# Kernel optimization log

Measured on AMD Instinct MI355X. Metric: run time of the kernel, lower is better.

The kernel has to match this reference:

```python
import jax, jax.numpy as jnp
import numpy as np

# Pangu-Weather EarthSpecificBlock, layer-1 config
WZ, WH, WW = 2, 6, 12          # window size (z, lat, lon)
Z, H, W = 8, 91, 180           # token grid after patch embedding
C = 192                        # token dim
HEADS = 6
B = 1
PAD_TOP, PAD_BOT = 2, 3        # lat 91 -> 96 (CustomPad3d, centered)
ZP, HP, WP = 8, 96, 180        # padded grid
NWB = (ZP // WZ) * (HP // WH)  # 64 bias windows (z*lat)
N = WZ * WH * WW               # 144 tokens per window


def earth_position_index():
    zi = np.arange(WZ); zj = -np.arange(WZ) * WZ
    hi = np.arange(WH); hj = -np.arange(WH) * WH
    w = np.arange(WW)
    c1 = np.stack(np.meshgrid(zi, hi, w, indexing='ij')).reshape(3, -1)
    c2 = np.stack(np.meshgrid(zj, hj, w, indexing='ij')).reshape(3, -1)
    coords = (c1[:, :, None] - c2[:, None, :]).transpose(1, 2, 0).astype(np.int64)
    coords[:, :, 2] += WW - 1
    coords[:, :, 1] *= 2 * WW - 1
    coords[:, :, 0] *= (2 * WW - 1) * WH * WH
    return coords.sum(-1)  # (N, N) int indices into bias table

POS_IDX = jnp.asarray(earth_position_index())


def layer_norm(x, w, b, eps=1e-5):
    mu = x.mean(-1, keepdims=True)
    var = ((x - mu) ** 2).mean(-1, keepdims=True)
    return (x - mu) * jax.lax.rsqrt(var + eps) * w + b


def setup_inputs() -> dict:
    key = jax.random.key(0)
    ks = jax.random.split(key, 8)
    f = lambda k, s: jax.random.normal(k, s, jnp.float32) * 0.02
    return {
        "x": jax.random.normal(ks[0], (B, Z * H * W, C), jnp.float32),
        "qkv_w": f(ks[1], (3 * C, C)),
        "qkv_b": jnp.zeros((3 * C,), jnp.float32),
        "proj_w": f(ks[2], (C, C)),
        "proj_b": jnp.zeros((C,), jnp.float32),
        "bias_table": f(ks[3], ((2 * WW - 1) * WH * WH * WZ * WZ, NWB, HEADS)),
        "norm1_w": jnp.ones((C,), jnp.float32),
        "norm1_b": jnp.zeros((C,), jnp.float32),
        "norm2_w": jnp.ones((C,), jnp.float32),
        "norm2_b": jnp.zeros((C,), jnp.float32),
        "mlp_w1": f(ks[4], (4 * C, C)),
        "mlp_b1": jnp.zeros((4 * C,), jnp.float32),
        "mlp_w2": f(ks[5], (C, 4 * C)),
        "mlp_b2": jnp.zeros((C,), jnp.float32),
        "roll": 0,
    }


def reference(x, qkv_w, qkv_b, proj_w, proj_b, bias_table,
              norm1_w, norm1_b, norm2_w, norm2_b,
              mlp_w1, mlp_b1, mlp_w2, mlp_b2, roll):
    shortcut = x  # (B, L, C)
    hd = C // HEADS
    scale = hd ** -0.5
    xs = x.reshape(B, Z, H, W, C)
    xs = jnp.pad(xs, ((0, 0), (0, 0), (PAD_TOP, PAD_BOT), (0, 0), (0, 0)))
    # window partition: (B, ZP, HP, WP, C) -> (nb, N, C), windows ordered (z, lat, lon)
    xw = xs.reshape(B, ZP // WZ, WZ, HP // WH, WH, WP // WW, WW, C)
    xw = xw.transpose(0, 1, 3, 5, 2, 4, 6, 7).reshape(-1, N, C)
    nb = xw.shape[0]  # B * 64 * 15 = 960
    qkv = (xw @ qkv_w.T + qkv_b).reshape(nb, N, 3, HEADS, hd).transpose(2, 0, 3, 1, 4)
    q, k, v = qkv[0] * scale, qkv[1], qkv[2]  # each (nb, HEADS, N, hd)
    att = jnp.einsum('bhnd,bhmd->bhnm', q, k)  # (nb, HEADS, N, N)
    # earth-specific bias gathered via position index
    bias = bias_table[POS_IDX]                 # (N, N, NWB, HEADS)
    bias = bias.transpose(2, 3, 0, 1)          # (NWB, HEADS, N, N)
    # nb = B * NWB * n_lon_windows, NWB is the leading window factor
    att = att.reshape(B, NWB, -1, HEADS, N, N) + bias[None, :, None]
    att = jax.nn.softmax(att, axis=-1).reshape(nb, HEADS, N, N)
    out = jnp.einsum('bhnm,bhmd->bnhd', att, v).reshape(nb, N, C)
    out = out @ proj_w.T + proj_b
    # window reverse + crop padding
    out = out.reshape(B, ZP // WZ, HP // WH, WP // WW, WZ, WH, WW, C)
    out = out.transpose(0, 1, 4, 2, 5, 3, 6, 7).reshape(B, ZP, HP, WP, C)
    out = out[:, :, PAD_TOP:HP - PAD_BOT, :, :].reshape(B, -1, C)
    # post-norm residual (Pangu): x = shortcut + norm1(attn); x = x + norm2(mlp(x))
    x1 = shortcut + layer_norm(out, norm1_w, norm1_b)
    h1 = jax.nn.gelu(x1 @ mlp_w1.T + mlp_b1, approximate=False)
    mlp_out = h1 @ mlp_w2.T + mlp_b2
    return x1 + layer_norm(mlp_out, norm2_w, norm2_b)
```

## Files before the change

### kernel.cpp

```cpp
#include <hip/hip_runtime.h>
#include <hip/hip_bf16.h>

typedef __hip_bfloat16 bf16;
#define DEVI __device__ __forceinline__

typedef __bf16 bf16x8 __attribute__((ext_vector_type(8)));
typedef __bf16 bf16x4 __attribute__((ext_vector_type(4)));
typedef float  f32x4  __attribute__((ext_vector_type(4)));

DEVI float bf2f(bf16 v) { return __bfloat162float(v); }
DEVI bf16 f2bf(float v) { return __float2bfloat16(v); }

DEVI unsigned short bfbits(float x) {
    bf16 h = __float2bfloat16(x);
    return *reinterpret_cast<unsigned short*>(&h);
}
DEVI unsigned int pack2(float x, float y) {
    return (unsigned int)bfbits(x) | ((unsigned int)bfbits(y) << 16);
}
DEVI bf16x8 pack8(float4 lo, float4 hi) {
    union { unsigned int u[4]; bf16x8 v; } z;
    z.u[0] = pack2(lo.x, lo.y); z.u[1] = pack2(lo.z, lo.w);
    z.u[2] = pack2(hi.x, hi.y); z.u[3] = pack2(hi.z, hi.w);
    return z.v;
}
DEVI bf16x8 ld8h(const bf16* p) {
    bf16x4 lo = *(const bf16x4*)p;
    bf16x4 hi = *(const bf16x4*)(p + 4);
    return __builtin_shufflevector(lo, hi, 0, 1, 2, 3, 4, 5, 6, 7);
}

__global__ __launch_bounds__(256) void prep_attn_w(
    const float* __restrict__ qkv_w, const float* __restrict__ qkv_b,
    bf16* __restrict__ qkv_wb, float* __restrict__ qkv_bb)
{
    const float scale = 0.17677669529663687f;
    int idx = blockIdx.x * 256 + threadIdx.x;
    if (idx < 110592) {
        int c = idx % 192, d = idx / 192;
        int h = d / 96, q2 = d - h * 96, seg = q2 >> 5, rr = q2 & 31;
        float v = qkv_w[(size_t)(seg * 192 + h * 32 + rr) * 192 + c];
        if (seg == 0) v *= scale;
        qkv_wb[idx] = f2bf(v);
    }
    if (idx < 576) {
        int h = idx / 96, q2 = idx - h * 96, seg = q2 >> 5, rr = q2 & 31;
        float b = qkv_b[seg * 192 + h * 32 + rr];
        if (seg == 0) b *= scale;
        qkv_bb[idx] = b;
    }
}

__global__ __launch_bounds__(256) void prep_bias(
    const float* __restrict__ bias_table, bf16* __restrict__ biasT)
{
    int idx = blockIdx.x * 256 + threadIdx.x;
    if (idx >= 7962624) return;
    int t = idx % 144;
    int k = (idx / 144) % 144;
    int r2 = idx / 20736;
    int h = r2 % 6, wb = r2 / 6;
    int tzq = t / 72, thq = (t / 12) % 6, twq = t % 12;
    int tzk = k / 72, thk = (k / 12) % 6, twk = k % 12;
    int bidx = (tzq + 2 * tzk) * 828 + (thq + 6 * thk) * 23 + (twq - twk + 11);
    biasT[idx] = f2bf(bias_table[(size_t)(bidx * 64 + wb) * 6 + h]);
}

__global__ __launch_bounds__(256, 3) void attn_mfma_kernel(
    const float* __restrict__ x, const bf16* __restrict__ qkv_wb,
    const float* __restrict__ qkv_bb, const bf16* __restrict__ biasT,
    bf16* __restrict__ attn_out)
{
    __shared__ alignas(16) char sm[30976];
    bf16* Qs  = (bf16*)sm;
    bf16* Ks  = (bf16*)(sm + 10368);
    bf16* VTs = (bf16*)(sm + 20736);

    const int tid  = threadIdx.x;
    const int wave = tid >> 6;
    const int lane = tid & 63;
    const int quad = lane >> 4;
    const int l15  = lane & 15;

    const int bid     = blockIdx.x;
    const int logical = (bid & 7) * 720 + (bid >> 3);
    const int wi      = logical / 6;
    const int head    = logical % 6;
    const int ww_  = wi % 15;
    const int hw   = (wi / 15) % 16;
    const int zw   = wi / 240;
    const int wb   = zw * 16 + hw;

    for (int i = tid; i < 512; i += 256) {
        int d = i >> 4, c = i & 15;
        VTs[d * 160 + 144 + c] = f2bf(0.f);
    }

    bf16x8 af[3][6];
#pragma unroll
    for (int i = 0; i < 3; ++i) {
        int mt = wave + 4 * i;
        if (mt < 9) {
            int t  = mt * 16 + l15;
            int tz = t / 72, rr = t - tz * 72;
            int th = rr / 12, tw = rr - th * 12;
            int lat = hw * 6 + th - 2;
            bool valid = (lat >= 0 && lat < 91);
            size_t base = ((size_t)((zw * 2 + tz) * 91 + (valid ? lat : 0)) * 180
                           + ww_ * 12 + tw) * 192;
#pragma unroll
            for (int ks = 0; ks < 6; ++ks) {
                float4 lo = make_float4(0.f, 0.f, 0.f, 0.f);
                float4 hi = make_float4(0.f, 0.f, 0.f, 0.f);
                if (valid) {
                    lo = *(const float4*)(x + base + ks * 32 + quad * 8);
                    hi = *(const float4*)(x + base + ks * 32 + quad * 8 + 4);
                }
                af[i][ks] = pack8(lo, hi);
            }
        }
    }

    for (int nt = 0; nt < 6; ++nt) {
        const bf16* wrow = qkv_wb + (size_t)(head * 96 + nt * 16 + l15) * 192;
        bf16x8 bw[6];
#pragma unroll
        for (int ks = 0; ks < 6; ++ks)
            bw[ks] = *(const bf16x8*)(wrow + ks * 32 + quad * 8);
        float bias = qkv_bb[head * 96 + nt * 16 + l15];

        f32x4 acc[3];
#pragma unroll
        for (int i = 0; i < 3; ++i) acc[i] = (f32x4){0.f, 0.f, 0.f, 0.f};
#pragma unroll
        for (int ks = 0; ks < 6; ++ks)
#pragma unroll
            for (int i = 0; i < 3; ++i) {
                int mt = wave + 4 * i;
                if (mt < 9)
                    acc[i] = __builtin_amdgcn_mfma_f32_16x16x32_bf16(
                        af[i][ks], bw[ks], acc[i], 0, 0, 0);
            }
#pragma unroll
        for (int i = 0; i < 3; ++i) {
            int mt = wave + 4 * i;
            if (mt < 9) {
#pragma unroll
                for (int r = 0; r < 4; ++r) {
                    float v = acc[i][r] + bias;
                    int tok = mt * 16 + quad * 4 + r;
                    if (nt < 2)      Qs[tok * 36 + nt * 16 + l15] = f2bf(v);
                    else if (nt < 4) Ks[tok * 36 + (nt - 2) * 16 + l15] = f2bf(v);
                    else             VTs[((nt - 4) * 16 + l15) * 160 + tok] = f2bf(v);
                }
            }
        }
    }
    __syncthreads();

    bf16x8 qb[3];
#pragma unroll
    for (int i = 0; i < 3; ++i) {
        int nti = wave + 4 * i;
        if (nti < 9) qb[i] = ld8h(Qs + (nti * 16 + l15) * 36 + quad * 8);
    }
    f32x4 st[3][9];
#pragma unroll
    for (int mt = 0; mt < 9; ++mt) {
        bf16x8 ka = ld8h(Ks + (mt * 16 + l15) * 36 + quad * 8);
#pragma unroll
        for (int i = 0; i < 3; ++i) {
            int nti = wave + 4 * i;
            st[i][mt] = (f32x4){0.f, 0.f, 0.f, 0.f};
            if (nti < 9)
                st[i][mt] = __builtin_amdgcn_mfma_f32_16x16x32_bf16(
                    ka, qb[i], st[i][mt], 0, 0, 0);
        }
    }

    const bf16* bt = biasT + (size_t)(wb * 6 + head) * 20736;
#pragma unroll
    for (int i = 0; i < 3; ++i) {
        int nti = wave + 4 * i;
        if (nti < 9) {
#pragma unroll
            for (int mt = 0; mt < 9; ++mt)
#pragma unroll
                for (int r = 0; r < 4; ++r)
                    st[i][mt][r] += bf2f(bt[(mt * 16 + quad * 4 + r) * 144
                                            + nti * 16 + l15]);
        }
    }

#pragma unroll
    for (int i = 0; i < 3; ++i) {
        int nti = wave + 4 * i;
        if (nti < 9) {
            float mx = -1e30f;
#pragma unroll
            for (int mt = 0; mt < 9; ++mt)
#pragma unroll
                for (int r = 0; r < 4; ++r) mx = fmaxf(mx, st[i][mt][r]);
            mx = fmaxf(mx, __shfl_xor(mx, 16, 64));
            mx = fmaxf(mx, __shfl_xor(mx, 32, 64));
            float s = 0.f;
#pragma unroll
            for (int mt = 0; mt < 9; ++mt)
#pragma unroll
                for (int r = 0; r < 4; ++r) {
                    float e = __expf(st[i][mt][r] - mx);
                    st[i][mt][r] = e;
                    s += e;
                }
            s += __shfl_xor(s, 16, 64);
            s += __shfl_xor(s, 32, 64);
            float inv = 1.f / s;
#pragma unroll
            for (int mt = 0; mt < 9; ++mt)
#pragma unroll
                for (int r = 0; r < 4; ++r) st[i][mt][r] *= inv;
        }
    }

    f32x4 oa[3][2];
#pragma unroll
    for (int i = 0; i < 3; ++i)
#pragma unroll
        for (int n2 = 0; n2 < 2; ++n2) oa[i][n2] = (f32x4){0.f, 0.f, 0.f, 0.f};

#pragma unroll
    for (int i = 0; i < 3; ++i) {
        int nti = wave + 4 * i;
        if (nti < 9) {
#pragma unroll
            for (int ks = 0; ks < 5; ++ks) {
                unsigned A0 = pack2(st[i][2 * ks][0], st[i][2 * ks][1]);
                unsigned A1 = pack2(st[i][2 * ks][2], st[i][2 * ks][3]);
                unsigned B0 = 0u, B1 = 0u;
                if (ks < 4) {
                    B0 = pack2(st[i][2 * ks + 1][0], st[i][2 * ks + 1][1]);
                    B1 = pack2(st[i][2 * ks + 1][2], st[i][2 * ks + 1][3]);
                }
                bool lo2 = quad < 2;
                unsigned Z0 = lo2 ? A0 : B0, Z1 = lo2 ? A1 : B1;
                unsigned Y0 = lo2 ? B0 : A0, Y1 = lo2 ? B1 : A1;
                unsigned s16_0 = __shfl_xor((int)Z0, 16, 64);
                unsigned s16_1 = __shfl_xor((int)Z1, 16, 64);
                unsigned s32_0 = __shfl_xor((int)Y0, 32, 64);
                unsigned s32_1 = __shfl_xor((int)Y1, 32, 64);
                unsigned s48_0 = __shfl_xor((int)Y0, 48, 64);
                unsigned s48_1 = __shfl_xor((int)Y1, 48, 64);
                union { unsigned u[4]; bf16x8 v; } fr;
                fr.u[0] = (quad == 0) ? Z0 : (quad == 1) ? s48_0 : (quad == 2) ? s32_0 : s16_0;
                fr.u[1] = (quad == 0) ? Z1 : (quad == 1) ? s48_1 : (quad == 2) ? s32_1 : s16_1;
                fr.u[2] = (quad == 0) ? s16_0 : (quad == 1) ? s32_0 : (quad == 2) ? s48_0 : Z0;
                fr.u[3] = (quad == 0) ? s16_1 : (quad == 1) ? s32_1 : (quad == 2) ? s48_1 : Z1;
#pragma unroll
                for (int n2 = 0; n2 < 2; ++n2) {
                    bf16x8 vb = *(const bf16x8*)(VTs + (n2 * 16 + l15) * 160
                                                 + ks * 32 + quad * 8);
                    oa[i][n2] = __builtin_amdgcn_mfma_f32_16x16x32_bf16(
                        fr.v, vb, oa[i][n2], 0, 0, 0);
                }
            }
        }
    }

#pragma unroll
    for (int i = 0; i < 3; ++i) {
        int nti = wave + 4 * i;
        if (nti < 9) {
#pragma unroll
            for (int n2 = 0; n2 < 2; ++n2)
#pragma unroll
                for (int r = 0; r < 4; ++r) {
                    int tok = nti * 16 + quad * 4 + r;
                    attn_out[(size_t)(wi * 144 + tok) * 192 + (head << 5) + n2 * 16 + l15]
                        = f2bf(oa[i][n2][r]);
                }
        }
    }
}

__global__ __launch_bounds__(256, 2) void proj_mfma_kernel(
    const bf16* __restrict__ attn, const float* __restrict__ proj_w,
    const float* __restrict__ proj_b, const float* __restrict__ xin,
    const float* __restrict__ n1w, const float* __restrict__ n1b,
    bf16* __restrict__ x1out)
{
    __shared__ alignas(16) char sm[56320];
    bf16*  Xs     = (bf16*)sm;
    float* wsum   = (float*)(sm + 51200);
    float* wsq    = (float*)(sm + 53248);
    float* mean_s = (float*)(sm + 55296);
    float* rstd_s = (float*)(sm + 55808);

    const int tid  = threadIdx.x;
    const int wave = tid >> 6;
    const int lane = tid & 63;
    const int quad = lane >> 4;
    const int l15  = lane & 15;
    const long tok0 = (long)blockIdx.x * 128;
    const int colw = wave * 48;

    for (int i = tid; i < 128 * 24; i += 256) {
        int r = i / 24, c4 = i - r * 24;
        long l = tok0 + r;
        uint4 v = make_uint4(0u, 0u, 0u, 0u);
        if (l < 131040) {
            int li  = (int)l;
            int z   = li / 16380, rem = li - z * 16380;
            int lat = rem / 180, lon = rem - lat * 180;
            int latp = lat + 2;
            int zw = z >> 1, tz = z & 1;
            int hw = latp / 6, th = latp - hw * 6;
            int wwn = lon / 12, tw = lon - wwn * 12;
            int wi = (zw * 16 + hw) * 15 + wwn;
            int t  = (tz * 6 + th) * 12 + tw;
            v = *(const uint4*)(attn + (size_t)(wi * 144 + t) * 192 + c4 * 8);
        }
        *(uint4*)(Xs + r * 200 + c4 * 8) = v;
    }
    __syncthreads();

    f32x4 o[3][8];
#pragma unroll
    for (int nt = 0; nt < 3; ++nt)
#pragma unroll
        for (int mt = 0; mt < 8; ++mt)
            o[nt][mt] = (f32x4){0.f, 0.f, 0.f, 0.f};

#pragma unroll
    for (int ks = 0; ks < 6; ++ks) {
        bf16x8 wfr[3];
#pragma unroll
        for (int nt = 0; nt < 3; ++nt) {
            const float* wp = proj_w + (size_t)(colw + nt * 16 + l15) * 192
                            + ks * 32 + quad * 8;
            float4 lo = *(const float4*)wp;
            float4 hi = *(const float4*)(wp + 4);
            wfr[nt] = pack8(lo, hi);
        }
#pragma unroll
        for (int mt = 0; mt < 8; ++mt) {
            bf16x8 a = *(const bf16x8*)(Xs + (mt * 16 + l15) * 200 + ks * 32 + quad * 8);
#pragma unroll
            for (int nt = 0; nt < 3; ++nt)
                o[nt][mt] = __builtin_amdgcn_mfma_f32_16x16x32_bf16(
                    a, wfr[nt], o[nt][mt], 0, 0, 0);
        }
    }

    float pbv[3], gw[3], gb[3];
#pragma unroll
    for (int nt = 0; nt < 3; ++nt) {
        int c = colw + nt * 16 + l15;
        pbv[nt] = proj_b[c];
        gw[nt]  = n1w[c];
        gb[nt]  = n1b[c];
    }
#pragma unroll
    for (int nt = 0; nt < 3; ++nt)
#pragma unroll
        for (int mt = 0; mt < 8; ++mt)
#pragma unroll
            for (int r = 0; r < 4; ++r)
                o[nt][mt][r] += pbv[nt];

#pragma unroll
    for (int mt = 0; mt < 8; ++mt) {
#pragma unroll
        for (int r = 0; r < 4; ++r) {
            float p = o[0][mt][r] + o[1][mt][r] + o[2][mt][r];
            float q = o[0][mt][r] * o[0][mt][r] + o[1][mt][r] * o[1][mt][r]
                    + o[2][mt][r] * o[2][mt][r];
#pragma unroll
            for (int m_ = 1; m_ < 16; m_ <<= 1) {
                p += __shfl_xor(p, m_, 64);
                q += __shfl_xor(q, m_, 64);
            }
            if (l15 == 0) {
                int row = mt * 16 + quad * 4 + r;
                wsum[row * 4 + wave] = p;
                wsq [row * 4 + wave] = q;
            }
        }
    }
    __syncthreads();
    if (tid < 128) {
        float s  = wsum[tid * 4] + wsum[tid * 4 + 1] + wsum[tid * 4 + 2] + wsum[tid * 4 + 3];
        float ss = wsq [tid * 4] + wsq [tid * 4 + 1] + wsq [tid * 4 + 2] + wsq [tid * 4 + 3];
        float m = s * (1.f / 192.f);
        float var = ss * (1.f / 192.f) - m * m;
        mean_s[tid] = m;
        rstd_s[tid] = rsqrtf(fmaxf(var, 0.f) + 1e-5f);
    }
    __syncthreads();

#pragma unroll
    for (int mt = 0; mt < 8; ++mt) {
#pragma unroll
        for (int r = 0; r < 4; ++r) {
            int row = mt * 16 + quad * 4 + r;
            long tok = tok0 + row;
            if (tok < 131040) {
                float m = mean_s[row], rsd = rstd_s[row];
#pragma unroll
                for (int nt = 0; nt < 3; ++nt) {
                    int c = colw + nt * 16 + l15;
                    float val = (o[nt][mt][r] - m) * rsd * gw[nt] + gb[nt]
                              + xin[(size_t)tok * 192 + c];
                    x1out[(size_t)tok * 192 + c] = f2bf(val);
                }
            }
        }
    }
}

__global__ __launch_bounds__(256) void prep_weights(
    const float* __restrict__ w1, const float* __restrict__ w2,
    unsigned int* __restrict__ w1b, unsigned int* __restrict__ w2b)
{
    int i = blockIdx.x * 256 + threadIdx.x;
    if (i < 73728) {
        w1b[i] = pack2(w1[2 * i], w1[2 * i + 1]);
    } else {
        int j = i - 73728;
        w2b[j] = pack2(w2[2 * j], w2[2 * j + 1]);
    }
}

__global__ __launch_bounds__(256, 2) void mlp_mfma_kernel(
    const bf16* __restrict__ x1, const bf16* __restrict__ w1b,
    const float* __restrict__ b1, const bf16* __restrict__ w2b,
    const float* __restrict__ b2, const float* __restrict__ n2w,
    const float* __restrict__ n2b, float* __restrict__ out)
{
    __shared__ alignas(16) char sm[53760];
    bf16*  Xs     = (bf16*)sm;
    bf16*  Hs     = (bf16*)(sm + 25600);
    float* wsum   = (float*)(sm + 51200);
    float* wsq    = (float*)(sm + 52224);
    float* mean_s = (float*)(sm + 53248);
    float* rstd_s = (float*)(sm + 53504);

    const int tid  = threadIdx.x;
    const int wave = tid >> 6;
    const int lane = tid & 63;
    const int quad = lane >> 4;
    const int l15  = lane & 15;
    const long tok0 = (long)blockIdx.x * 64;
    const int colw = wave * 48;

    for (int i = tid; i < 64 * 24; i += 256) {
        int r = i / 24, c8 = i - r * 24;
        uint4 v = make_uint4(0u, 0u, 0u, 0u);
        if (tok0 + r < 131040)
            v = *(const uint4*)(x1 + (tok0 + r) * 192 + (size_t)c8 * 8);
        *(uint4*)(Xs + r * 200 + c8 * 8) = v;
    }
    __syncthreads();

    bf16x8 af[4][6];
#pragma unroll
    for (int mt = 0; mt < 4; ++mt)
#pragma unroll
        for (int ks = 0; ks < 6; ++ks)
            af[mt][ks] = *(const bf16x8*)(Xs + (mt * 16 + l15) * 200 + ks * 32 + quad * 8);

    f32x4 o[3][4];
#pragma unroll
    for (int nt = 0; nt < 3; ++nt)
#pragma unroll
        for (int mt = 0; mt < 4; ++mt)
            o[nt][mt] = (f32x4){0.f, 0.f, 0.f, 0.f};

    for (int nc = 0; nc < 4; ++nc) {
        f32x4 g[3][4];
#pragma unroll
        for (int nt = 0; nt < 3; ++nt)
#pragma unroll
            for (int mt = 0; mt < 4; ++mt)
                g[nt][mt] = (f32x4){0.f, 0.f, 0.f, 0.f};
        const int h0 = nc * 192 + colw;
#pragma unroll
        for (int ks = 0; ks < 6; ++ks) {
            bf16x8 bfr[3];
#pragma unroll
            for (int nt = 0; nt < 3; ++nt)
                bfr[nt] = *(const bf16x8*)(w1b + (size_t)(h0 + nt * 16 + l15) * 192 + ks * 32 + quad * 8);
#pragma unroll
            for (int nt = 0; nt < 3; ++nt)
#pragma unroll
                for (int mt = 0; mt < 4; ++mt)
                    g[nt][mt] = __builtin_amdgcn_mfma_f32_16x16x32_bf16(
                        af[mt][ks], bfr[nt], g[nt][mt], 0, 0, 0);
        }
        __syncthreads();

#pragma unroll
        for (int nt = 0; nt < 3; ++nt) {
            float bb = b1[h0 + nt * 16 + l15];
            int hcol = colw + nt * 16 + l15;
#pragma unroll
            for (int mt = 0; mt < 4; ++mt) {
#pragma unroll
                for (int r = 0; r < 4; ++r) {
                    float v = g[nt][mt][r] + bb;
                    float u = v * (0.7978845608028654f + 0.035677408136300125f * v * v);
                    float e = __expf(2.f * u);
                    float t = 1.f - 2.f / (e + 1.f);
                    float gl = 0.5f * v * (1.f + t);
                    Hs[(mt * 16 + quad * 4 + r) * 200 + hcol] = f2bf(gl);
                }
            }
        }
        __syncthreads();

#pragma unroll
        for (int ks = 0; ks < 6; ++ks) {
            bf16x8 hf[4];
#pragma unroll
            for (int mt = 0; mt < 4; ++mt)
                hf[mt] = *(const bf16x8*)(Hs + (mt * 16 + l15) * 200 + ks * 32 + quad * 8);
            bf16x8 wf[3];
#pragma unroll
            for (int nt = 0; nt < 3; ++nt)
                wf[nt] = *(const bf16x8*)(w2b + (size_t)(colw + nt * 16 + l15) * 768 + nc * 192 + ks * 32 + quad * 8);
#pragma unroll
            for (int nt = 0; nt < 3; ++nt)
#pragma unroll
                for (int mt = 0; mt < 4; ++mt)
                    o[nt][mt] = __builtin_amdgcn_mfma_f32_16x16x32_bf16(
                        hf[mt], wf[nt], o[nt][mt], 0, 0, 0);
        }
    }

    float b2v[3], gw[3], gb[3];
#pragma unroll
    for (int nt = 0; nt < 3; ++nt) {
        int c = colw + nt * 16 + l15;
        b2v[nt] = b2[c];
        gw[nt] = n2w[c];
        gb[nt] = n2b[c];
    }
#pragma unroll
    for (int nt = 0; nt < 3; ++nt)
#pragma unroll
        for (int mt = 0; mt < 4; ++mt)
#pragma unroll
            for (int r = 0; r < 4; ++r)
                o[nt][mt][r] += b2v[nt];

#pragma unroll
    for (int mt = 0; mt < 4; ++mt) {
#pragma unroll
        for (int r = 0; r < 4; ++r) {
            float p = o[0][mt][r] + o[1][mt][r] + o[2][mt][r];
            float q = o[0][mt][r] * o[0][mt][r] + o[1][mt][r] * o[1][mt][r]
                    + o[2][mt][r] * o[2][mt][r];
#pragma unroll
            for (int m_ = 1; m_ < 16; m_ <<= 1) {
                p += __shfl_xor(p, m_, 64);
                q += __shfl_xor(q, m_, 64);
            }
            if (l15 == 0) {
                int row = mt * 16 + quad * 4 + r;
                wsum[row * 4 + wave] = p;
                wsq [row * 4 + wave] = q;
            }
        }
    }
    __syncthreads();
    if (tid < 64) {
        float s  = wsum[tid * 4] + wsum[tid * 4 + 1] + wsum[tid * 4 + 2] + wsum[tid * 4 + 3];
        float ss = wsq [tid * 4] + wsq [tid * 4 + 1] + wsq [tid * 4 + 2] + wsq [tid * 4 + 3];
        float m = s * (1.f / 192.f);
        float var = ss * (1.f / 192.f) - m * m;
        mean_s[tid] = m;
        rstd_s[tid] = rsqrtf(fmaxf(var, 0.f) + 1e-5f);
    }
    __syncthreads();

#pragma unroll
    for (int mt = 0; mt < 4; ++mt) {
#pragma unroll
        for (int r = 0; r < 4; ++r) {
            int row = mt * 16 + quad * 4 + r;
            long tok = tok0 + row;
            if (tok < 131040) {
                float m = mean_s[row], rsd = rstd_s[row];
#pragma unroll
                for (int nt = 0; nt < 3; ++nt) {
                    int c = colw + nt * 16 + l15;
                    float val = (o[nt][mt][r] - m) * rsd * gw[nt] + gb[nt]
                              + bf2f(Xs[row * 200 + c]);
                    out[tok * 192 + c] = val;
                }
            }
        }
    }
}

extern "C" void kernel_launch(void* const* d_in, const int* in_sizes, int n_in,
                              void* d_out, int out_size, void* d_ws, size_t ws_size,
                              hipStream_t stream) {
    (void)in_sizes; (void)n_in; (void)out_size; (void)ws_size;
    const float* x          = (const float*)d_in[0];
    const float* qkv_w      = (const float*)d_in[1];
    const float* qkv_b      = (const float*)d_in[2];
    const float* proj_w     = (const float*)d_in[3];
    const float* proj_b     = (const float*)d_in[4];
    const float* bias_table = (const float*)d_in[5];
    const float* n1w        = (const float*)d_in[6];
    const float* n1b        = (const float*)d_in[7];
    const float* n2w        = (const float*)d_in[8];
    const float* n2b        = (const float*)d_in[9];
    const float* w1         = (const float*)d_in[10];
    const float* b1         = (const float*)d_in[11];
    const float* w2         = (const float*)d_in[12];
    const float* b2         = (const float*)d_in[13];
    float* out = (float*)d_out;

    bf16*  attn_ws = (bf16*)d_ws;
    bf16*  x1_ws   = (bf16*)((char*)d_ws + 53084160);
    bf16*  w1b     = (bf16*)d_ws;
    bf16*  w2b     = (bf16*)((char*)d_ws + 294912);
    bf16*  qkv_wb  = (bf16*)((char*)d_ws + 53084160);
    float* qkv_bb  = (float*)((char*)d_ws + 53305344);
    bf16*  biasT   = (bf16*)((char*)d_ws + 53307648);

    prep_attn_w<<<432, 256, 0, stream>>>(qkv_w, qkv_b, qkv_wb, qkv_bb);
    prep_bias<<<31104, 256, 0, stream>>>(bias_table, biasT);
    attn_mfma_kernel<<<5760, 256, 0, stream>>>(x, qkv_wb, qkv_bb, biasT, attn_ws);
    proj_mfma_kernel<<<1024, 256, 0, stream>>>(attn_ws, proj_w, proj_b, x, n1w, n1b, x1_ws);
    prep_weights<<<576, 256, 0, stream>>>(w1, w2, (unsigned int*)w1b, (unsigned int*)w2b);
    mlp_mfma_kernel<<<2048, 256, 0, stream>>>(x1_ws, w1b, b1, w2b, b2, n2w, n2b, out);
}
```

Baseline: 783.6 us.

## Process one query tile at a time in attention to cut register pressure

Restructures the attention kernel so each wave handles its up-to-three row tiles one after another, not all at once. The QKV projection, the score/softmax and the PV stages each now live inside a per-tile loop, which shrinks the live accumulator arrays. Launch bounds rise from 3 to 4 blocks per CU to use the freed registers for occupancy. The cost is that the QKV weight fragments are reloaded once per tile and there is less instruction-level parallelism between independent MFMA chains.

Result: faster. 756.2 us (-3.5%).

```diff
diff --git a/kernel.cpp b/kernel.cpp
--- a/kernel.cpp
+++ b/kernel.cpp
@@ -66,7 +66,7 @@
     biasT[idx] = f2bf(bias_table[(size_t)(bidx * 64 + wb) * 6 + h]);
 }
 
-__global__ __launch_bounds__(256, 3) void attn_mfma_kernel(
+__global__ __launch_bounds__(256, 4) void attn_mfma_kernel(
     const float* __restrict__ x, const bf16* __restrict__ qkv_wb,
     const float* __restrict__ qkv_bb, const bf16* __restrict__ biasT,
     bf16* __restrict__ attn_out)
@@ -96,8 +96,6 @@
         VTs[d * 160 + 144 + c] = f2bf(0.f);
     }
 
-    bf16x8 af[3][6];
-#pragma unroll
     for (int i = 0; i < 3; ++i) {
         int mt = wave + 4 * i;
         if (mt < 9) {
@@ -108,6 +106,7 @@
             bool valid = (lat >= 0 && lat < 91);
             size_t base = ((size_t)((zw * 2 + tz) * 91 + (valid ? lat : 0)) * 180
                            + ww_ * 12 + tw) * 192;
+            bf16x8 af[6];
 #pragma unroll
             for (int ks = 0; ks < 6; ++ks) {
                 float4 lo = make_float4(0.f, 0.f, 0.f, 0.f);
@@ -116,38 +115,24 @@
                     lo = *(const float4*)(x + base + ks * 32 + quad * 8);
                     hi = *(const float4*)(x + base + ks * 32 + quad * 8 + 4);
                 }
-                af[i][ks] = pack8(lo, hi);
-            }
-        }
-    }
-
-    for (int nt = 0; nt < 6; ++nt) {
-        const bf16* wrow = qkv_wb + (size_t)(head * 96 + nt * 16 + l15) * 192;
-        bf16x8 bw[6];
-#pragma unroll
-        for (int ks = 0; ks < 6; ++ks)
-            bw[ks] = *(const bf16x8*)(wrow + ks * 32 + quad * 8);
-        float bias = qkv_bb[head * 96 + nt * 16 + l15];
-
-        f32x4 acc[3];
-#pragma unroll
-        for (int i = 0; i < 3; ++i) acc[i] = (f32x4){0.f, 0.f, 0.f, 0.f};
-#pragma unroll
-        for (int ks = 0; ks < 6; ++ks)
-#pragma unroll
-            for (int i = 0; i < 3; ++i) {
-                int mt = wave + 4 * i;
-                if (mt < 9)
-                    acc[i] = __builtin_amdgcn_mfma_f32_16x16x32_bf16(
-                        af[i][ks], bw[ks], acc[i], 0, 0, 0);
-            }
-#pragma unroll
-        for (int i = 0; i < 3; ++i) {
-            int mt = wave + 4 * i;
-            if (mt < 9) {
+                af[ks] = pack8(lo, hi);
+            }
+            for (int nt = 0; nt < 6; ++nt) {
+                const bf16* wrow = qkv_wb + (size_t)(head * 96 + nt * 16 + l15) * 192;
+                bf16x8 bw[6];
+#pragma unroll
+                for (int ks = 0; ks < 6; ++ks)
+                    bw[ks] = *(const bf16x8*)(wrow + ks * 32 + quad * 8);
+                float bias = qkv_bb[head * 96 + nt * 16 + l15];
+
+                f32x4 acc = (f32x4){0.f, 0.f, 0.f, 0.f};
+#pragma unroll
+                for (int ks = 0; ks < 6; ++ks)
+                    acc = __builtin_amdgcn_mfma_f32_16x16x32_bf16(
+                        af[ks], bw[ks], acc, 0, 0, 0);
 #pragma unroll
                 for (int r = 0; r < 4; ++r) {
-                    float v = acc[i][r] + bias;
+                    float v = acc[r] + bias;
                     int tok = mt * 16 + quad * 4 + r;
                     if (nt < 2)      Qs[tok * 36 + nt * 16 + l15] = f2bf(v);
                     else if (nt < 4) Ks[tok * 36 + (nt - 2) * 16 + l15] = f2bf(v);
@@ -158,127 +143,97 @@
     }
     __syncthreads();
 
-    bf16x8 qb[3];
-#pragma unroll
+    const bf16* bt = biasT + (size_t)(wb * 6 + head) * 20736;
+
     for (int i = 0; i < 3; ++i) {
         int nti = wave + 4 * i;
-        if (nti < 9) qb[i] = ld8h(Qs + (nti * 16 + l15) * 36 + quad * 8);
-    }
-    f32x4 st[3][9];
-#pragma unroll
-    for (int mt = 0; mt < 9; ++mt) {
-        bf16x8 ka = ld8h(Ks + (mt * 16 + l15) * 36 + quad * 8);
-#pragma unroll
-        for (int i = 0; i < 3; ++i) {
-            int nti = wave + 4 * i;
-            st[i][mt] = (f32x4){0.f, 0.f, 0.f, 0.f};
-            if (nti < 9)
-                st[i][mt] = __builtin_amdgcn_mfma_f32_16x16x32_bf16(
-                    ka, qb[i], st[i][mt], 0, 0, 0);
-        }
-    }
-
-    const bf16* bt = biasT + (size_t)(wb * 6 + head) * 20736;
-#pragma unroll
-    for (int i = 0; i < 3; ++i) {
-        int nti = wave + 4 * i;
-        if (nti < 9) {
-#pragma unroll
-            for (int mt = 0; mt < 9; ++mt)
-#pragma unroll
-                for (int r = 0; r < 4; ++r)
-                    st[i][mt][r] += bf2f(bt[(mt * 16 + quad * 4 + r) * 144
-                                            + nti * 16 + l15]);
-        }
-    }
-
-#pragma unroll
-    for (int i = 0; i < 3; ++i) {
-        int nti = wave + 4 * i;
-        if (nti < 9) {
-            float mx = -1e30f;
-#pragma unroll
-            for (int mt = 0; mt < 9; ++mt)
-#pragma unroll
-                for (int r = 0; r < 4; ++r) mx = fmaxf(mx, st[i][mt][r]);
-            mx = fmaxf(mx, __shfl_xor(mx, 16, 64));
-            mx = fmaxf(mx, __shfl_xor(mx, 32, 64));
-            float s = 0.f;
-#pragma unroll
-            for (int mt = 0; mt < 9; ++mt)
-#pragma unroll
-                for (int r = 0; r < 4; ++r) {
-                    float e = __expf(st[i][mt][r] - mx);
-                    st[i][mt][r] = e;
-                    s += e;
-                }
-            s += __shfl_xor(s, 16, 64);
-            s += __shfl_xor(s, 32, 64);
-            float inv = 1.f / s;
-#pragma unroll
-            for (int mt = 0; mt < 9; ++mt)
-#pragma unroll
-                for (int r = 0; r < 4; ++r) st[i][mt][r] *= inv;
-        }
-    }
-
-    f32x4 oa[3][2];
-#pragma unroll
-    for (int i = 0; i < 3; ++i)
-#pragma unroll
-        for (int n2 = 0; n2 < 2; ++n2) oa[i][n2] = (f32x4){0.f, 0.f, 0.f, 0.f};
-
-#pragma unroll
-    for (int i = 0; i < 3; ++i) {
-        int nti = wave + 4 * i;
-        if (nti < 9) {
-#pragma unroll
-            for (int ks = 0; ks < 5; ++ks) {
-                unsigned A0 = pack2(st[i][2 * ks][0], st[i][2 * ks][1]);
-                unsigned A1 = pack2(st[i][2 * ks][2], st[i][2 * ks][3]);
-                unsigned B0 = 0u, B1 = 0u;
-                if (ks < 4) {
-                    B0 = pack2(st[i][2 * ks + 1][0], st[i][2 * ks + 1][1]);
-                    B1 = pack2(st[i][2 * ks + 1][2], st[i][2 * ks + 1][3]);
-                }
-                bool lo2 = quad < 2;
-                unsigned Z0 = lo2 ? A0 : B0, Z1 = lo2 ? A1 : B1;
-                unsigned Y0 = lo2 ? B0 : A0, Y1 = lo2 ? B1 : A1;
-                unsigned s16_0 = __shfl_xor((int)Z0, 16, 64);
-                unsigned s16_1 = __shfl_xor((int)Z1, 16, 64);
-                unsigned s32_0 = __shfl_xor((int)Y0, 32, 64);
-                unsigned s32_1 = __shfl_xor((int)Y1, 32, 64);
-                unsigned s48_0 = __shfl_xor((int)Y0, 48, 64);
-                unsigned s48_1 = __shfl_xor((int)Y1, 48, 64);
-                union { unsigned u[4]; bf16x8 v; } fr;
-                fr.u[0] = (quad == 0) ? Z0 : (quad == 1) ? s48_0 : (quad == 2) ? s32_0 : s16_0;
-                fr.u[1] = (quad == 0) ? Z1 : (quad == 1) ? s48_1 : (quad == 2) ? s32_1 : s16_1;
-                fr.u[2] = (quad == 0) ? s16_0 : (quad == 1) ? s32_0 : (quad == 2) ? s48_0 : Z0;
-                fr.u[3] = (quad == 0) ? s16_1 : (quad == 1) ? s32_1 : (quad == 2) ? s48_1 : Z1;
-#pragma unroll
-                for (int n2 = 0; n2 < 2; ++n2) {
-                    bf16x8 vb = *(const bf16x8*)(VTs + (n2 * 16 + l15) * 160
-                                                 + ks * 32 + quad * 8);
-                    oa[i][n2] = __builtin_amdgcn_mfma_f32_16x16x32_bf16(
-                        fr.v, vb, oa[i][n2], 0, 0, 0);
-                }
-            }
-        }
-    }
-
-#pragma unroll
-    for (int i = 0; i < 3; ++i) {
-        int nti = wave + 4 * i;
-        if (nti < 9) {
-#pragma unroll
-            for (int n2 = 0; n2 < 2; ++n2)
-#pragma unroll
-                for (int r = 0; r < 4; ++r) {
-                    int tok = nti * 16 + quad * 4 + r;
-                    attn_out[(size_t)(wi * 144 + tok) * 192 + (head << 5) + n2 * 16 + l15]
-                        = f2bf(oa[i][n2][r]);
-                }
-        }
+        if (nti >= 9) continue;
+
+        bf16x8 qb = ld8h(Qs + (nti * 16 + l15) * 36 + quad * 8);
+
+        f32x4 st[9];
+#pragma unroll
+        for (int mt = 0; mt < 9; ++mt) {
+            bf16x8 ka = ld8h(Ks + (mt * 16 + l15) * 36 + quad * 8);
+            st[mt] = (f32x4){0.f, 0.f, 0.f, 0.f};
+            st[mt] = __builtin_amdgcn_mfma_f32_16x16x32_bf16(
+                ka, qb, st[mt], 0, 0, 0);
+        }
+
+#pragma unroll
+        for (int mt = 0; mt < 9; ++mt)
+#pragma unroll
+            for (int r = 0; r < 4; ++r)
+                st[mt][r] += bf2f(bt[(mt * 16 + quad * 4 + r) * 144
+                                     + nti * 16 + l15]);
+
+        float mx = -1e30f;
+#pragma unroll
+        for (int mt = 0; mt < 9; ++mt)
+#pragma unroll
+            for (int r = 0; r < 4; ++r) mx = fmaxf(mx, st[mt][r]);
+        mx = fmaxf(mx, __shfl_xor(mx, 16, 64));
+        mx = fmaxf(mx, __shfl_xor(mx, 32, 64));
+        float s = 0.f;
+#pragma unroll
+        for (int mt = 0; mt < 9; ++mt)
+#pragma unroll
+            for (int r = 0; r < 4; ++r) {
+                float e = __expf(st[mt][r] - mx);
+                st[mt][r] = e;
+                s += e;
+            }
+        s += __shfl_xor(s, 16, 64);
+        s += __shfl_xor(s, 32, 64);
+        float inv = 1.f / s;
+#pragma unroll
+        for (int mt = 0; mt < 9; ++mt)
+#pragma unroll
+            for (int r = 0; r < 4; ++r) st[mt][r] *= inv;
+
+        f32x4 oa[2];
+        oa[0] = (f32x4){0.f, 0.f, 0.f, 0.f};
+        oa[1] = (f32x4){0.f, 0.f, 0.f, 0.f};
+#pragma unroll
+        for (int ks = 0; ks < 5; ++ks) {
+            unsigned A0 = pack2(st[2 * ks][0], st[2 * ks][1]);
+            unsigned A1 = pack2(st[2 * ks][2], st[2 * ks][3]);
+            unsigned B0 = 0u, B1 = 0u;
+            if (ks < 4) {
+                B0 = pack2(st[2 * ks + 1][0], st[2 * ks + 1][1]);
+                B1 = pack2(st[2 * ks + 1][2], st[2 * ks + 1][3]);
+            }
+            bool lo2 = quad < 2;
+            unsigned Z0 = lo2 ? A0 : B0, Z1 = lo2 ? A1 : B1;
+            unsigned Y0 = lo2 ? B0 : A0, Y1 = lo2 ? B1 : A1;
+            unsigned s16_0 = __shfl_xor((int)Z0, 16, 64);
+            unsigned s16_1 = __shfl_xor((int)Z1, 16, 64);
+            unsigned s32_0 = __shfl_xor((int)Y0, 32, 64);
+            unsigned s32_1 = __shfl_xor((int)Y1, 32, 64);
+            unsigned s48_0 = __shfl_xor((int)Y0, 48, 64);
+            unsigned s48_1 = __shfl_xor((int)Y1, 48, 64);
+            union { unsigned u[4]; bf16x8 v; } fr;
+            fr.u[0] = (quad == 0) ? Z0 : (quad == 1) ? s48_0 : (quad == 2) ? s32_0 : s16_0;
+            fr.u[1] = (quad == 0) ? Z1 : (quad == 1) ? s48_1 : (quad == 2) ? s32_1 : s16_1;
+            fr.u[2] = (quad == 0) ? s16_0 : (quad == 1) ? s32_0 : (quad == 2) ? s48_0 : Z0;
+            fr.u[3] = (quad == 0) ? s16_1 : (quad == 1) ? s32_1 : (quad == 2) ? s48_1 : Z1;
+#pragma unroll
+            for (int n2 = 0; n2 < 2; ++n2) {
+                bf16x8 vb = *(const bf16x8*)(VTs + (n2 * 16 + l15) * 160
+                                             + ks * 32 + quad * 8);
+                oa[n2] = __builtin_amdgcn_mfma_f32_16x16x32_bf16(
+                    fr.v, vb, oa[n2], 0, 0, 0);
+            }
+        }
+
+#pragma unroll
+        for (int n2 = 0; n2 < 2; ++n2)
+#pragma unroll
+            for (int r = 0; r < 4; ++r) {
+                int tok = nti * 16 + quad * 4 + r;
+                attn_out[(size_t)(wi * 144 + tok) * 192 + (head << 5) + n2 * 16 + l15]
+                    = f2bf(oa[n2][r]);
+            }
     }
 }
 
```
